# Kernel optimization log

Hardware: AMD Instinct MI355X
Metric: run time of the kernel (lower is better)

The kernel has to match this reference:

```python
import jax, jax.numpy as jnp
import numpy as np

H = 1024        # hidden_size
NH = 16         # num_attention_heads
HD = H // NH    # attention_head_size = 64
EPS = 1e-12


def setup_inputs() -> dict:
    key = jax.random.key(0)
    ks = jax.random.split(key, 12)
    B, S = 2, 2048
    s = 0.02
    return {
        "hidden_states": jax.random.normal(ks[0], (B, S, H), jnp.float32),
        "attention_mask": jnp.zeros((B, 1, 1, S), jnp.float32),
        "Wq": jax.random.normal(ks[1], (H, H), jnp.float32) * s,
        "bq": jnp.zeros((H,), jnp.float32),
        "Wk": jax.random.normal(ks[2], (H, H), jnp.float32) * s,
        "bk": jnp.zeros((H,), jnp.float32),
        "Wv": jax.random.normal(ks[3], (H, H), jnp.float32) * s,
        "bv": jnp.zeros((H,), jnp.float32),
        "Wd": jax.random.normal(ks[4], (H, H), jnp.float32) * s,
        "bd": jnp.zeros((H,), jnp.float32),
        "ln_gamma": jnp.ones((H,), jnp.float32),
        "ln_beta": jnp.zeros((H,), jnp.float32),
    }


def _split_heads(x):
    # [B,S,H] -> [B,NH,S,HD]
    B, S, _ = x.shape
    return x.reshape(B, S, NH, HD).transpose(0, 2, 1, 3)


def reference(hidden_states, attention_mask, Wq, bq, Wk, bk, Wv, bv, Wd, bd, ln_gamma, ln_beta):
    q = _split_heads(hidden_states @ Wq.T + bq)
    k = _split_heads(hidden_states @ Wk.T + bk)
    v = _split_heads(hidden_states @ Wv.T + bv)

    scores = jnp.einsum("bhqd,bhkd->bhqk", q, k) / jnp.sqrt(jnp.float32(HD))
    scores = scores + attention_mask
    probs = jax.nn.softmax(scores, axis=-1)  # attention dropout p=0

    ctx = jnp.einsum("bhqk,bhkd->bhqd", probs, v)
    B, _, S, _ = ctx.shape
    ctx = ctx.transpose(0, 2, 1, 3).reshape(B, S, H)

    proj = ctx @ Wd.T + bd  # output dropout p=0
    x = hidden_states + proj
    mu = jnp.mean(x, axis=-1, keepdims=True)
    var = jnp.mean(jnp.square(x - mu), axis=-1, keepdims=True)
    out = (x - mu) * jax.lax.rsqrt(var + EPS) * ln_gamma + ln_beta
    return out
```

## Files before the change

kernel.cpp:

```cpp
#include <hip/hip_runtime.h>

typedef unsigned short u16;
typedef __attribute__((ext_vector_type(4))) unsigned short u16x4;
typedef __attribute__((ext_vector_type(8))) unsigned short u16x8;
typedef __attribute__((ext_vector_type(8))) __bf16 bf16x8;
typedef __attribute__((ext_vector_type(4))) float f32x4;

#define S_LEN 2048
#define HDIM 1024
#define NHEAD 16
#define HD 64
#define MTOK 4096
#define QKV_STRIDE 4194304
#define LOG2E 1.44269504089f
#define QKSCL (0.125f * 1.44269504089f)

__device__ __forceinline__ float bf2f(u16 h) {
    unsigned u = ((unsigned)h) << 16;
    return __builtin_bit_cast(float, u);
}
__device__ __forceinline__ u16 f2bf(float f) {
    return __builtin_bit_cast(u16, (__bf16)f);
}
__device__ __forceinline__ bf16x8 as_bf16(u16x8 u) {
    union { u16x8 a; bf16x8 b; } c; c.a = u; return c.b;
}
__device__ __forceinline__ void gld_lds16(const u16* g, u16* l) {
    __builtin_amdgcn_global_load_lds((const __attribute__((address_space(1))) u16*)g,
                                     (__attribute__((address_space(3))) u16*)l, 16, 0, 0);
}

__device__ __forceinline__ void cast4(const float* __restrict__ s, u16* __restrict__ d, int i) {
    f32x4 v = *(const f32x4*)(s + (size_t)i * 4);
    u16x4 o;
    o[0] = f2bf(v[0]); o[1] = f2bf(v[1]); o[2] = f2bf(v[2]); o[3] = f2bf(v[3]);
    *(u16x4*)(d + (size_t)i * 4) = o;
}

__global__ __launch_bounds__(256) void prep(const float* __restrict__ hs,
                                            const float* __restrict__ Wq, const float* __restrict__ Wk,
                                            const float* __restrict__ Wv, const float* __restrict__ Wd,
                                            const float* __restrict__ bq, const float* __restrict__ bk,
                                            const float* __restrict__ bv,
                                            u16* __restrict__ hsb, u16* __restrict__ wqkvb,
                                            u16* __restrict__ wdb, float* __restrict__ b3) {
    int bid = blockIdx.x, tid = threadIdx.x;
    if (bid < 4096) {
        cast4(hs, hsb, bid * 256 + tid);
    } else if (bid < 5120) {
        cast4(Wq, wqkvb, (bid - 4096) * 256 + tid);
    } else if (bid < 6144) {
        cast4(Wk, wqkvb + HDIM * HDIM, (bid - 5120) * 256 + tid);
    } else if (bid < 7168) {
        cast4(Wv, wqkvb + 2 * HDIM * HDIM, (bid - 6144) * 256 + tid);
    } else if (bid < 8192) {
        cast4(Wd, wdb, (bid - 7168) * 256 + tid);
    } else {
        int i = (bid - 8192) * 256 + tid;
        if (i < 3072) b3[i] = (i < 1024) ? bq[i] : (i < 2048) ? bk[i - 1024] : bv[i - 2048];
    }
}

template <int MODE>
__global__ __launch_bounds__(256, 2) void gemm_bt(const u16* __restrict__ A, const u16* __restrict__ Bw,
                                                  const float* __restrict__ bias,
                                                  u16* __restrict__ outb, u16* __restrict__ vtout,
                                                  float* __restrict__ outf,
                                                  int Md, int Nd, int Kd) {
    __shared__ alignas(16) u16 As[128 * 32];
    __shared__ alignas(16) u16 Bs[128 * 32];
    const int tid = threadIdx.x;
    const int wave = tid >> 6, lane = tid & 63;
    const int l15 = lane & 15, l4 = lane >> 4;
    const int m0 = blockIdx.y * 128, n0 = blockIdx.x * 128;
    const int wm = wave >> 1, wn = wave & 1;

    f32x4 acc[4][4];
#pragma unroll
    for (int i = 0; i < 4; i++)
#pragma unroll
        for (int j = 0; j < 4; j++) acc[i][j] = (f32x4){0.f, 0.f, 0.f, 0.f};

    for (int k0 = 0; k0 < Kd; k0 += 32) {
#pragma unroll
        for (int i = 0; i < 2; i++) {
            int cc = wave * 2 + i;
            int row = cc * 16 + (lane >> 2);
            int co = (lane & 3) * 8;
            gld_lds16(A + (size_t)(m0 + row) * Kd + k0 + co, &As[cc * 512]);
            gld_lds16(Bw + (size_t)(n0 + row) * Kd + k0 + co, &Bs[cc * 512]);
        }
        __syncthreads();
        bf16x8 af[4], bf[4];
#pragma unroll
        for (int x = 0; x < 4; x++) {
            af[x] = as_bf16(*(const u16x8*)&As[(wm * 64 + x * 16 + l15) * 32 + l4 * 8]);
            bf[x] = as_bf16(*(const u16x8*)&Bs[(wn * 64 + x * 16 + l15) * 32 + l4 * 8]);
        }
#pragma unroll
        for (int mi = 0; mi < 4; mi++)
#pragma unroll
            for (int nj = 0; nj < 4; nj++)
                acc[mi][nj] = __builtin_amdgcn_mfma_f32_16x16x32_bf16(af[mi], bf[nj], acc[mi][nj], 0, 0, 0);
        __syncthreads();
    }

#pragma unroll
    for (int mi = 0; mi < 4; mi++) {
#pragma unroll
        for (int nj = 0; nj < 4; nj++) {
            int coln = n0 + wn * 64 + nj * 16 + l15;
            float bv_ = bias[coln];
            int rowb = m0 + wm * 64 + mi * 16 + l4 * 4;
            if (MODE == 0) {
                int which = coln >> 10, nn = coln & 1023;
                int hh = nn >> 6, dd = nn & 63;
                int bb = rowb >> 11, ss = rowb & 2047;
                if (which < 2) {
#pragma unroll
                    for (int r = 0; r < 4; r++)
                        outb[(size_t)which * QKV_STRIDE + ((size_t)((bb << 4) + hh) * S_LEN + ss + r) * HD + dd] =
                            f2bf(acc[mi][nj][r] + bv_);
                } else {
                    u16x4 o;
#pragma unroll
                    for (int r = 0; r < 4; r++) o[r] = f2bf(acc[mi][nj][r] + bv_);
                    *(u16x4*)(vtout + ((size_t)((bb << 4) + hh) * HD + dd) * S_LEN + ss) = o;
                }
            } else {
#pragma unroll
                for (int r = 0; r < 4; r++)
                    outf[(size_t)(rowb + r) * Nd + coln] = acc[mi][nj][r] + bv_;
            }
        }
    }
}

__global__ __launch_bounds__(512, 4) void flash_attn3(const u16* __restrict__ qkv,
                                                      const u16* __restrict__ vt,
                                                      const float* __restrict__ amask,
                                                      u16* __restrict__ ctx) {
    __shared__ alignas(16) u16 Kb[3][4096];
    __shared__ alignas(16) u16 Vb[3][4096];
    __shared__ alignas(16) u16 Pl[8][1024];
    __shared__ float Ml[2048];

    const int tid = threadIdx.x;
    const int wave = tid >> 6, lane = tid & 63;
    const int l15 = lane & 15, l4 = lane >> 4;
    const int lid = blockIdx.x;
    const int idx = lid >> 3;
    const int bh = (lid & 7) * 4 + (idx >> 4);
    const int qx = idx & 15;
    const int b = bh >> 4, h = bh & 15;
    const int qr0 = qx * 128 + wave * 16;

    const u16* qh = qkv + (size_t)bh * (S_LEN * HD);
    const u16* kh = qh + QKV_STRIDE;
    const u16* vth = vt + (size_t)bh * (S_LEN * HD);
    u16* pw = &Pl[wave][0];

    {
        f32x4 m = *(const f32x4*)(amask + (size_t)b * S_LEN + tid * 4);
        f32x4 mm;
#pragma unroll
        for (int j = 0; j < 4; j++) mm[j] = m[j] * LOG2E;
        *(f32x4*)&Ml[tid * 4] = mm;
    }

    bf16x8 qf[2];
#pragma unroll
    for (int ks = 0; ks < 2; ks++)
        qf[ks] = as_bf16(*(const u16x8*)(qh + (size_t)(qr0 + l15) * HD + ks * 32 + l4 * 8));

    __syncthreads();

    const int srow = lane >> 3;
    const int schunk = (lane & 7) ^ srow;
    const int krow = wave * 8 + srow;
    const u16* ksrc = kh + (size_t)krow * HD + schunk * 8;
    const u16* vsrc = vth + (size_t)krow * S_LEN + schunk * 8;

    f32x4 acc_o[4];
    float l_run = 0.f;
#pragma unroll
    for (int x = 0; x < 4; x++) acc_o[x] = (f32x4){0.f, 0.f, 0.f, 0.f};

    auto STAGE = [&](int T, int buf) {
        gld_lds16(ksrc + (size_t)T * 64 * HD, &Kb[buf][wave * 512]);
        gld_lds16(vsrc + T * 64, &Vb[buf][wave * 512]);
    };

    auto tile = [&](int t, int buf) {
        const u16* kb = &Kb[buf][0];
        const u16* vb = &Vb[buf][0];
        f32x4 accs[4];
#pragma unroll
        for (int nj = 0; nj < 4; nj++) accs[nj] = (f32x4){0.f, 0.f, 0.f, 0.f};
        __builtin_amdgcn_s_setprio(1);
#pragma unroll
        for (int ks = 0; ks < 2; ks++) {
            bf16x8 kf[4];
#pragma unroll
            for (int nj = 0; nj < 4; nj++) {
                int n = nj * 16 + l15;
                kf[nj] = as_bf16(*(const u16x8*)&kb[n * 64 + ((ks * 32 + l4 * 8) ^ ((n & 7) << 3))]);
            }
#pragma unroll
            for (int nj = 0; nj < 4; nj++)
                accs[nj] = __builtin_amdgcn_mfma_f32_16x16x32_bf16(kf[nj], qf[ks], accs[nj], 0, 0, 0);
        }
        __builtin_amdgcn_s_setprio(0);
        const int kv0 = t * 64;
        const int rsw = (l15 & 7) << 3;
#pragma unroll
        for (int nj = 0; nj < 4; nj++) {
            f32x4 mk = *(const f32x4*)&Ml[kv0 + nj * 16 + l4 * 4];
            u16x4 o;
#pragma unroll
            for (int r = 0; r < 4; r++) {
                float p = __builtin_amdgcn_exp2f(accs[nj][r] * QKSCL + mk[r]);
                l_run += p;
                o[r] = f2bf(p);
            }
            *(u16x4*)&pw[l15 * 64 + ((nj * 16 + l4 * 4) ^ rsw)] = o;
        }
        __builtin_amdgcn_s_setprio(1);
#pragma unroll
        for (int ks = 0; ks < 2; ks++) {
            int kvoff = ks * 32 + l4 * 8;
            bf16x8 pf = as_bf16(*(const u16x8*)&pw[l15 * 64 + (kvoff ^ rsw)]);
            bf16x8 vf[4];
#pragma unroll
            for (int dj = 0; dj < 4; dj++) {
                int d = dj * 16 + l15;
                vf[dj] = as_bf16(*(const u16x8*)&vb[d * 64 + (kvoff ^ ((d & 7) << 3))]);
            }
#pragma unroll
            for (int dj = 0; dj < 4; dj++)
                acc_o[dj] = __builtin_amdgcn_mfma_f32_16x16x32_bf16(vf[dj], pf, acc_o[dj], 0, 0, 0);
        }
        __builtin_amdgcn_s_setprio(0);
    };

    STAGE(0, 0);
    STAGE(1, 1);

    for (int t = 0; t < 30; ++t) {
        __builtin_amdgcn_s_barrier();
        STAGE(t + 2, (t + 2) % 3);
        asm volatile("s_waitcnt vmcnt(4)" ::: "memory");
        __builtin_amdgcn_s_barrier();
        tile(t, t % 3);
    }
    __builtin_amdgcn_s_barrier();
    asm volatile("s_waitcnt vmcnt(2)" ::: "memory");
    __builtin_amdgcn_s_barrier();
    tile(30, 0);
    __builtin_amdgcn_s_barrier();
    asm volatile("s_waitcnt vmcnt(0)" ::: "memory");
    __builtin_amdgcn_s_barrier();
    tile(31, 1);

    float l = l_run;
    l += __shfl_xor(l, 16);
    l += __shfl_xor(l, 32);
    float inv = 1.0f / l;
    u16* cp = ctx + ((size_t)b * S_LEN + qr0 + l15) * HDIM + h * HD + l4 * 4;
#pragma unroll
    for (int dj = 0; dj < 4; dj++) {
        u16x4 o;
#pragma unroll
        for (int r = 0; r < 4; r++) o[r] = f2bf(acc_o[dj][r] * inv);
        *(u16x4*)(cp + dj * 16) = o;
    }
}

__global__ __launch_bounds__(256) void resid_ln(const float* __restrict__ hs, const float* __restrict__ proj,
                                                const float* __restrict__ g, const float* __restrict__ be,
                                                float* __restrict__ out) {
    int row = blockIdx.x, tid = threadIdx.x;
    int base = row * HDIM + tid * 4;
    f32x4 a = *(const f32x4*)(hs + base);
    f32x4 p = *(const f32x4*)(proj + base);
    f32x4 x = a + p;
    float s = x[0] + x[1] + x[2] + x[3];
    float sq = x[0] * x[0] + x[1] * x[1] + x[2] * x[2] + x[3] * x[3];
#pragma unroll
    for (int m = 1; m < 64; m <<= 1) {
        s += __shfl_xor(s, m);
        sq += __shfl_xor(sq, m);
    }
    __shared__ float red[8];
    int wave = tid >> 6, lane = tid & 63;
    if (lane == 0) { red[wave] = s; red[4 + wave] = sq; }
    __syncthreads();
    s = red[0] + red[1] + red[2] + red[3];
    sq = red[4] + red[5] + red[6] + red[7];
    float mean = s * (1.0f / 1024.0f);
    float var = sq * (1.0f / 1024.0f) - mean * mean;
    float rstd = rsqrtf(fmaxf(var, 0.f) + 1e-12f);
    f32x4 gg = *(const f32x4*)(g + tid * 4);
    f32x4 bb = *(const f32x4*)(be + tid * 4);
    f32x4 o;
#pragma unroll
    for (int j = 0; j < 4; j++) o[j] = (x[j] - mean) * rstd * gg[j] + bb[j];
    *(f32x4*)(out + base) = o;
}

extern "C" void kernel_launch(void* const* d_in, const int* in_sizes, int n_in,
                              void* d_out, int out_size, void* d_ws, size_t ws_size,
                              hipStream_t stream) {
    const float* hs    = (const float*)d_in[0];
    const float* amask = (const float*)d_in[1];
    const float* Wq    = (const float*)d_in[2];
    const float* bq    = (const float*)d_in[3];
    const float* Wk    = (const float*)d_in[4];
    const float* bk    = (const float*)d_in[5];
    const float* Wv    = (const float*)d_in[6];
    const float* bv    = (const float*)d_in[7];
    const float* Wd    = (const float*)d_in[8];
    const float* bd    = (const float*)d_in[9];
    const float* gamma = (const float*)d_in[10];
    const float* beta  = (const float*)d_in[11];

    char* ws = (char*)d_ws;
    u16*   hsb   = (u16*)(ws);
    u16*   Wqkvb = (u16*)(ws + ((size_t)8 << 20));
    u16*   Wdb   = (u16*)(ws + ((size_t)14 << 20));
    u16*   qkv   = (u16*)(ws + ((size_t)16 << 20));
    u16*   vt    = qkv + 2 * (size_t)QKV_STRIDE;
    u16*   ctx   = (u16*)(ws + ((size_t)40 << 20));
    float* proj  = (float*)(ws + ((size_t)48 << 20));
    float* b3    = (float*)(ws + ((size_t)64 << 20));

    prep<<<8204, 256, 0, stream>>>(hs, Wq, Wk, Wv, Wd, bq, bk, bv, hsb, Wqkvb, Wdb, b3);

    gemm_bt<0><<<dim3(24, 32), 256, 0, stream>>>(hsb, Wqkvb, b3, qkv, vt, nullptr, MTOK, 3072, HDIM);

    flash_attn3<<<512, 512, 0, stream>>>(qkv, vt, amask, ctx);

    gemm_bt<1><<<dim3(8, 32), 256, 0, stream>>>(ctx, Wdb, bd, nullptr, nullptr, proj, MTOK, HDIM, HDIM);

    resid_ln<<<MTOK, 256, 0, stream>>>(hs, proj, gamma, beta, (float*)d_out);
}
```

Measured before the change: 127.8 us.

## Load K/V tiles directly into registers in attention, drop LDS staging and barriers

The attention kernel stops staging K and V tiles through shared memory with a triple-buffered async pipeline and barriers. Each wave now loads its MFMA operand fragments straight from global memory into registers, prefetching the next tile after the current one is used. Blocks shrink to 4 waves covering 64 query rows, launched as 1024 blocks. This removes LDS traffic and block-wide synchronisation, but every wave re-reads K/V from global/L2 with no sharing and no swizzled coalescing, and register pressure rises.

```diff
diff --git a/kernel.cpp b/kernel.cpp
--- a/kernel.cpp
+++ b/kernel.cpp
@@ -136,36 +136,36 @@
     }
 }
 
-__global__ __launch_bounds__(512, 4) void flash_attn3(const u16* __restrict__ qkv,
+__global__ __launch_bounds__(256, 4) void flash_attn4(const u16* __restrict__ qkv,
                                                       const u16* __restrict__ vt,
                                                       const float* __restrict__ amask,
                                                       u16* __restrict__ ctx) {
-    __shared__ alignas(16) u16 Kb[3][4096];
-    __shared__ alignas(16) u16 Vb[3][4096];
-    __shared__ alignas(16) u16 Pl[8][1024];
     __shared__ float Ml[2048];
+    __shared__ alignas(16) u16 Pl[4][1024];
 
     const int tid = threadIdx.x;
     const int wave = tid >> 6, lane = tid & 63;
     const int l15 = lane & 15, l4 = lane >> 4;
     const int lid = blockIdx.x;
     const int idx = lid >> 3;
-    const int bh = (lid & 7) * 4 + (idx >> 4);
-    const int qx = idx & 15;
+    const int bh = (lid & 7) * 4 + (idx >> 5);
+    const int qt = idx & 31;
     const int b = bh >> 4, h = bh & 15;
-    const int qr0 = qx * 128 + wave * 16;
+    const int qr0 = qt * 64 + wave * 16;
 
     const u16* qh = qkv + (size_t)bh * (S_LEN * HD);
     const u16* kh = qh + QKV_STRIDE;
     const u16* vth = vt + (size_t)bh * (S_LEN * HD);
     u16* pw = &Pl[wave][0];
+    const int rsw = (l15 & 7) << 3;
 
     {
-        f32x4 m = *(const f32x4*)(amask + (size_t)b * S_LEN + tid * 4);
-        f32x4 mm;
-#pragma unroll
-        for (int j = 0; j < 4; j++) mm[j] = m[j] * LOG2E;
-        *(f32x4*)&Ml[tid * 4] = mm;
+        f32x4 m0 = *(const f32x4*)(amask + (size_t)b * S_LEN + tid * 8);
+        f32x4 m1 = *(const f32x4*)(amask + (size_t)b * S_LEN + tid * 8 + 4);
+#pragma unroll
+        for (int j = 0; j < 4; j++) { m0[j] *= LOG2E; m1[j] *= LOG2E; }
+        *(f32x4*)&Ml[tid * 8] = m0;
+        *(f32x4*)&Ml[tid * 8 + 4] = m1;
     }
 
     bf16x8 qf[2];
@@ -175,44 +175,47 @@
 
     __syncthreads();
 
-    const int srow = lane >> 3;
-    const int schunk = (lane & 7) ^ srow;
-    const int krow = wave * 8 + srow;
-    const u16* ksrc = kh + (size_t)krow * HD + schunk * 8;
-    const u16* vsrc = vth + (size_t)krow * S_LEN + schunk * 8;
-
     f32x4 acc_o[4];
     float l_run = 0.f;
 #pragma unroll
     for (int x = 0; x < 4; x++) acc_o[x] = (f32x4){0.f, 0.f, 0.f, 0.f};
-
-    auto STAGE = [&](int T, int buf) {
-        gld_lds16(ksrc + (size_t)T * 64 * HD, &Kb[buf][wave * 512]);
-        gld_lds16(vsrc + T * 64, &Vb[buf][wave * 512]);
+    const f32x4 zed = (f32x4){0.f, 0.f, 0.f, 0.f};
+
+    u16x8 kreg[8], vreg[8];
+    auto LOADK = [&](int t) {
+        int kv0 = (t & 31) * 64;
+#pragma unroll
+        for (int ks = 0; ks < 2; ks++)
+#pragma unroll
+            for (int nj = 0; nj < 4; nj++)
+                kreg[ks * 4 + nj] = *(const u16x8*)(kh + ((size_t)(kv0 + nj * 16 + l15) << 6) + ks * 32 + l4 * 8);
     };
-
-    auto tile = [&](int t, int buf) {
-        const u16* kb = &Kb[buf][0];
-        const u16* vb = &Vb[buf][0];
+    auto LOADV = [&](int t) {
+        int kv0 = (t & 31) * 64;
+#pragma unroll
+        for (int ks = 0; ks < 2; ks++)
+#pragma unroll
+            for (int dj = 0; dj < 4; dj++)
+                vreg[ks * 4 + dj] = *(const u16x8*)(vth + ((size_t)(dj * 16 + l15) << 11) + kv0 + ks * 32 + l4 * 8);
+    };
+
+    LOADK(0);
+    LOADV(0);
+
+    for (int t = 0; t < 32; ++t) {
+        const int kv0 = t * 64;
         f32x4 accs[4];
-#pragma unroll
-        for (int nj = 0; nj < 4; nj++) accs[nj] = (f32x4){0.f, 0.f, 0.f, 0.f};
         __builtin_amdgcn_s_setprio(1);
 #pragma unroll
-        for (int ks = 0; ks < 2; ks++) {
-            bf16x8 kf[4];
-#pragma unroll
-            for (int nj = 0; nj < 4; nj++) {
-                int n = nj * 16 + l15;
-                kf[nj] = as_bf16(*(const u16x8*)&kb[n * 64 + ((ks * 32 + l4 * 8) ^ ((n & 7) << 3))]);
-            }
-#pragma unroll
-            for (int nj = 0; nj < 4; nj++)
-                accs[nj] = __builtin_amdgcn_mfma_f32_16x16x32_bf16(kf[nj], qf[ks], accs[nj], 0, 0, 0);
-        }
+        for (int nj = 0; nj < 4; nj++)
+            accs[nj] = __builtin_amdgcn_mfma_f32_16x16x32_bf16(as_bf16(kreg[nj]), qf[0], zed, 0, 0, 0);
+#pragma unroll
+        for (int nj = 0; nj < 4; nj++)
+            accs[nj] = __builtin_amdgcn_mfma_f32_16x16x32_bf16(as_bf16(kreg[4 + nj]), qf[1], accs[nj], 0, 0, 0);
         __builtin_amdgcn_s_setprio(0);
-        const int kv0 = t * 64;
-        const int rsw = (l15 & 7) << 3;
+
+        LOADK(t + 1);
+
 #pragma unroll
         for (int nj = 0; nj < 4; nj++) {
             f32x4 mk = *(const f32x4*)&Ml[kv0 + nj * 16 + l4 * 4];
@@ -225,42 +228,20 @@
             }
             *(u16x4*)&pw[l15 * 64 + ((nj * 16 + l4 * 4) ^ rsw)] = o;
         }
+
         __builtin_amdgcn_s_setprio(1);
 #pragma unroll
         for (int ks = 0; ks < 2; ks++) {
             int kvoff = ks * 32 + l4 * 8;
             bf16x8 pf = as_bf16(*(const u16x8*)&pw[l15 * 64 + (kvoff ^ rsw)]);
-            bf16x8 vf[4];
-#pragma unroll
-            for (int dj = 0; dj < 4; dj++) {
-                int d = dj * 16 + l15;
-                vf[dj] = as_bf16(*(const u16x8*)&vb[d * 64 + (kvoff ^ ((d & 7) << 3))]);
-            }
 #pragma unroll
             for (int dj = 0; dj < 4; dj++)
-                acc_o[dj] = __builtin_amdgcn_mfma_f32_16x16x32_bf16(vf[dj], pf, acc_o[dj], 0, 0, 0);
+                acc_o[dj] = __builtin_amdgcn_mfma_f32_16x16x32_bf16(as_bf16(vreg[ks * 4 + dj]), pf, acc_o[dj], 0, 0, 0);
         }
         __builtin_amdgcn_s_setprio(0);
-    };
-
-    STAGE(0, 0);
-    STAGE(1, 1);
-
-    for (int t = 0; t < 30; ++t) {
-        __builtin_amdgcn_s_barrier();
-        STAGE(t + 2, (t + 2) % 3);
-        asm volatile("s_waitcnt vmcnt(4)" ::: "memory");
-        __builtin_amdgcn_s_barrier();
-        tile(t, t % 3);
-    }
-    __builtin_amdgcn_s_barrier();
-    asm volatile("s_waitcnt vmcnt(2)" ::: "memory");
-    __builtin_amdgcn_s_barrier();
-    tile(30, 0);
-    __builtin_amdgcn_s_barrier();
-    asm volatile("s_waitcnt vmcnt(0)" ::: "memory");
-    __builtin_amdgcn_s_barrier();
-    tile(31, 1);
+
+        LOADV(t + 1);
+    }
 
     float l = l_run;
     l += __shfl_xor(l, 16);
@@ -338,7 +319,7 @@
 
     gemm_bt<0><<<dim3(24, 32), 256, 0, stream>>>(hsb, Wqkvb, b3, qkv, vt, nullptr, MTOK, 3072, HDIM);
 
-    flash_attn3<<<512, 512, 0, stream>>>(qkv, vt, amask, ctx);
+    flash_attn4<<<1024, 256, 0, stream>>>(qkv, vt, amask, ctx);
 
     gemm_bt<1><<<dim3(8, 32), 256, 0, stream>>>(ctx, Wdb, bd, nullptr, nullptr, proj, MTOK, HDIM, HDIM);
 
```

Measured after the change: 317.6 us. 148% more time.

## Double-buffer GEMM LDS loads and shrink attention LDS for higher occupancy

Applied to the files above, without the earlier changes.

The GEMM now double-buffers its A/B LDS tiles, issuing the next K-slice's global-to-LDS loads before computing the current one, with raw barriers, vmcnt waits and raised MFMA priority. The flash attention kernel moves from triple to double buffering of K/V and stores the attention mask as bf16 instead of fp32. Together with higher launch-bounds occupancy hints, this cuts LDS per block so more blocks can be resident per CU. The risks are less prefetch depth in attention, register pressure from the tighter occupancy bounds, and a bf16-rounded mask that is lossless only for zero/large-negative masks.

```diff
diff --git a/kernel.cpp b/kernel.cpp
--- a/kernel.cpp
+++ b/kernel.cpp
@@ -62,47 +62,65 @@
 }
 
 template <int MODE>
-__global__ __launch_bounds__(256, 2) void gemm_bt(const u16* __restrict__ A, const u16* __restrict__ Bw,
+__global__ __launch_bounds__(256, 3) void gemm_bt(const u16* __restrict__ A, const u16* __restrict__ Bw,
                                                   const float* __restrict__ bias,
                                                   u16* __restrict__ outb, u16* __restrict__ vtout,
                                                   float* __restrict__ outf,
                                                   int Md, int Nd, int Kd) {
-    __shared__ alignas(16) u16 As[128 * 32];
-    __shared__ alignas(16) u16 Bs[128 * 32];
+    __shared__ alignas(16) u16 As[2][128 * 32];
+    __shared__ alignas(16) u16 Bs[2][128 * 32];
     const int tid = threadIdx.x;
     const int wave = tid >> 6, lane = tid & 63;
     const int l15 = lane & 15, l4 = lane >> 4;
     const int m0 = blockIdx.y * 128, n0 = blockIdx.x * 128;
     const int wm = wave >> 1, wn = wave & 1;
 
+    const int cc0 = wave * 2;
+    const int srow = lane >> 2;
+    const int sco = (lane & 3) * 8;
+
     f32x4 acc[4][4];
 #pragma unroll
     for (int i = 0; i < 4; i++)
 #pragma unroll
         for (int j = 0; j < 4; j++) acc[i][j] = (f32x4){0.f, 0.f, 0.f, 0.f};
 
-    for (int k0 = 0; k0 < Kd; k0 += 32) {
+    auto STAGE = [&](int k0, int buf) {
 #pragma unroll
         for (int i = 0; i < 2; i++) {
-            int cc = wave * 2 + i;
-            int row = cc * 16 + (lane >> 2);
-            int co = (lane & 3) * 8;
-            gld_lds16(A + (size_t)(m0 + row) * Kd + k0 + co, &As[cc * 512]);
-            gld_lds16(Bw + (size_t)(n0 + row) * Kd + k0 + co, &Bs[cc * 512]);
-        }
-        __syncthreads();
+            int cc = cc0 + i;
+            int row = cc * 16 + srow;
+            gld_lds16(A + (size_t)(m0 + row) * Kd + k0 + sco, &As[buf][cc * 512]);
+            gld_lds16(Bw + (size_t)(n0 + row) * Kd + k0 + sco, &Bs[buf][cc * 512]);
+        }
+    };
+
+    const int nt = Kd >> 5;
+    STAGE(0, 0);
+    for (int t = 0; t < nt; ++t) {
+        __builtin_amdgcn_s_barrier();
+        if (t + 1 < nt) {
+            STAGE((t + 1) << 5, (t + 1) & 1);
+            asm volatile("s_waitcnt vmcnt(4)" ::: "memory");
+        } else {
+            asm volatile("s_waitcnt vmcnt(0)" ::: "memory");
+        }
+        __builtin_amdgcn_s_barrier();
+        const u16* as = &As[t & 1][0];
+        const u16* bs = &Bs[t & 1][0];
         bf16x8 af[4], bf[4];
 #pragma unroll
         for (int x = 0; x < 4; x++) {
-            af[x] = as_bf16(*(const u16x8*)&As[(wm * 64 + x * 16 + l15) * 32 + l4 * 8]);
-            bf[x] = as_bf16(*(const u16x8*)&Bs[(wn * 64 + x * 16 + l15) * 32 + l4 * 8]);
-        }
+            af[x] = as_bf16(*(const u16x8*)&as[(wm * 64 + x * 16 + l15) * 32 + l4 * 8]);
+            bf[x] = as_bf16(*(const u16x8*)&bs[(wn * 64 + x * 16 + l15) * 32 + l4 * 8]);
+        }
+        __builtin_amdgcn_s_setprio(1);
 #pragma unroll
         for (int mi = 0; mi < 4; mi++)
 #pragma unroll
             for (int nj = 0; nj < 4; nj++)
                 acc[mi][nj] = __builtin_amdgcn_mfma_f32_16x16x32_bf16(af[mi], bf[nj], acc[mi][nj], 0, 0, 0);
-        __syncthreads();
+        __builtin_amdgcn_s_setprio(0);
     }
 
 #pragma unroll
@@ -136,14 +154,14 @@
     }
 }
 
-__global__ __launch_bounds__(512, 4) void flash_attn3(const u16* __restrict__ qkv,
+__global__ __launch_bounds__(512, 6) void flash_attn5(const u16* __restrict__ qkv,
                                                       const u16* __restrict__ vt,
                                                       const float* __restrict__ amask,
                                                       u16* __restrict__ ctx) {
-    __shared__ alignas(16) u16 Kb[3][4096];
-    __shared__ alignas(16) u16 Vb[3][4096];
+    __shared__ alignas(16) u16 Kb[2][4096];
+    __shared__ alignas(16) u16 Vb[2][4096];
     __shared__ alignas(16) u16 Pl[8][1024];
-    __shared__ float Ml[2048];
+    __shared__ u16 Mlb[2048];
 
     const int tid = threadIdx.x;
     const int wave = tid >> 6, lane = tid & 63;
@@ -162,10 +180,10 @@
 
     {
         f32x4 m = *(const f32x4*)(amask + (size_t)b * S_LEN + tid * 4);
-        f32x4 mm;
-#pragma unroll
-        for (int j = 0; j < 4; j++) mm[j] = m[j] * LOG2E;
-        *(f32x4*)&Ml[tid * 4] = mm;
+        u16x4 mm;
+#pragma unroll
+        for (int j = 0; j < 4; j++) mm[j] = f2bf(m[j] * LOG2E);
+        *(u16x4*)&Mlb[tid * 4] = mm;
     }
 
     bf16x8 qf[2];
@@ -215,11 +233,11 @@
         const int rsw = (l15 & 7) << 3;
 #pragma unroll
         for (int nj = 0; nj < 4; nj++) {
-            f32x4 mk = *(const f32x4*)&Ml[kv0 + nj * 16 + l4 * 4];
+            u16x4 mraw = *(const u16x4*)&Mlb[kv0 + nj * 16 + l4 * 4];
             u16x4 o;
 #pragma unroll
             for (int r = 0; r < 4; r++) {
-                float p = __builtin_amdgcn_exp2f(accs[nj][r] * QKSCL + mk[r]);
+                float p = __builtin_amdgcn_exp2f(accs[nj][r] * QKSCL + bf2f(mraw[r]));
                 l_run += p;
                 o[r] = f2bf(p);
             }
@@ -244,23 +262,17 @@
     };
 
     STAGE(0, 0);
-    STAGE(1, 1);
-
-    for (int t = 0; t < 30; ++t) {
+    for (int t = 0; t < 32; ++t) {
         __builtin_amdgcn_s_barrier();
-        STAGE(t + 2, (t + 2) % 3);
-        asm volatile("s_waitcnt vmcnt(4)" ::: "memory");
+        if (t + 1 < 32) {
+            STAGE(t + 1, (t + 1) & 1);
+            asm volatile("s_waitcnt vmcnt(2)" ::: "memory");
+        } else {
+            asm volatile("s_waitcnt vmcnt(0)" ::: "memory");
+        }
         __builtin_amdgcn_s_barrier();
-        tile(t, t % 3);
-    }
-    __builtin_amdgcn_s_barrier();
-    asm volatile("s_waitcnt vmcnt(2)" ::: "memory");
-    __builtin_amdgcn_s_barrier();
-    tile(30, 0);
-    __builtin_amdgcn_s_barrier();
-    asm volatile("s_waitcnt vmcnt(0)" ::: "memory");
-    __builtin_amdgcn_s_barrier();
-    tile(31, 1);
+        tile(t, t & 1);
+    }
 
     float l = l_run;
     l += __shfl_xor(l, 16);
@@ -338,7 +350,7 @@
 
     gemm_bt<0><<<dim3(24, 32), 256, 0, stream>>>(hsb, Wqkvb, b3, qkv, vt, nullptr, MTOK, 3072, HDIM);
 
-    flash_attn3<<<512, 512, 0, stream>>>(qkv, vt, amask, ctx);
+    flash_attn5<<<512, 512, 0, stream>>>(qkv, vt, amask, ctx);
 
     gemm_bt<1><<<dim3(8, 32), 256, 0, stream>>>(ctx, Wdb, bd, nullptr, nullptr, proj, MTOK, HDIM, HDIM);
 
```

After: 128.4 us. Within noise of the previous version (+0.5%).
